# Performance work log

Hardware: AMD Instinct MI355X
Metric: run time of the kernel (lower is better)

## Reference

```python
import jax, jax.numpy as jnp
import numpy as np

NEG_SLOPE = 0.2

def _gat(x_src, x_dst, W_src, W_dst, a_src, a_dst, bias, src, dst, num_dst):
    # Bipartite PyG GATConv, heads=1, concat, add_self_loops=False.
    h_src = x_src @ W_src              # [N_src, H]
    h_dst = x_dst @ W_dst              # [N_dst, H]
    # Per-edge attention logits: leaky_relu(a_src.h_src[i] + a_dst.h_dst[j])
    e = jax.nn.leaky_relu((h_src @ a_src)[src] + (h_dst @ a_dst)[dst], NEG_SLOPE)  # [E]
    # Segment softmax over incoming edges of each dst node
    m = jax.ops.segment_max(e, dst, num_segments=num_dst)
    m = jnp.where(jnp.isfinite(m), m, 0.0)  # empty segments -> safe
    ex = jnp.exp(e - m[dst])
    denom = jax.ops.segment_sum(ex, dst, num_segments=num_dst)
    alpha = ex / denom[dst]            # [E]
    # Scatter-sum weighted source messages
    out = jax.ops.segment_sum(alpha[:, None] * h_src[src], dst, num_segments=num_dst)
    return out + bias


def setup_inputs() -> dict:
    key = jax.random.key(0)
    ks = jax.random.split(key, 20)
    N_L, N_A, D, H, O, E = 100000, 20000, 128, 128, 64, 500000
    s = 1.0 / np.sqrt(D)
    inp = {
        'x_label': jax.random.normal(ks[0], (N_L, D), jnp.float32),
        'x_attr': jax.random.normal(ks[1], (N_A, D), jnp.float32),
        'W_src_la': jax.random.normal(ks[2], (D, H), jnp.float32) * s,
        'W_dst_la': jax.random.normal(ks[3], (D, H), jnp.float32) * s,
        'a_src_la': jax.random.normal(ks[4], (H,), jnp.float32) * s,
        'a_dst_la': jax.random.normal(ks[5], (H,), jnp.float32) * s,
        'b_la': jax.random.normal(ks[6], (H,), jnp.float32) * 0.01,
        'W_src_al': jax.random.normal(ks[7], (D, H), jnp.float32) * s,
        'W_dst_al': jax.random.normal(ks[8], (D, H), jnp.float32) * s,
        'a_src_al': jax.random.normal(ks[9], (H,), jnp.float32) * s,
        'a_dst_al': jax.random.normal(ks[10], (H,), jnp.float32) * s,
        'b_al': jax.random.normal(ks[11], (H,), jnp.float32) * 0.01,
        'W_lin': jax.random.normal(ks[12], (H, O), jnp.float32) * s,
        'b_lin': jax.random.normal(ks[13], (O,), jnp.float32) * 0.01,
        'edge_src_la': jax.random.randint(ks[14], (E,), 0, N_L, jnp.int32),
        'edge_dst_la': jax.random.randint(ks[15], (E,), 0, N_A, jnp.int32),
        'edge_src_al': jax.random.randint(ks[16], (E,), 0, N_A, jnp.int32),
        'edge_dst_al': jax.random.randint(ks[17], (E,), 0, N_L, jnp.int32),
    }
    return inp


def reference(x_label, x_attr, W_src_la, W_dst_la, a_src_la, a_dst_la, b_la,
              W_src_al, W_dst_al, a_src_al, a_dst_al, b_al, W_lin, b_lin,
              edge_src_la, edge_dst_la, edge_src_al, edge_dst_al):
    N_L = x_label.shape[0]
    N_A = x_attr.shape[0]
    # label -> attribute GAT (output for 'attribute' nodes)
    h_attr = _gat(x_label, x_attr, W_src_la, W_dst_la, a_src_la, a_dst_la, b_la,
                  edge_src_la, edge_dst_la, N_A)
    # attribute -> label GAT (output for 'label' nodes)
    h_label = _gat(x_attr, x_label, W_src_al, W_dst_al, a_src_al, a_dst_al, b_al,
                   edge_src_al, edge_dst_al, N_L)
    h_attr = jax.nn.relu(h_attr)  # computed as in original (unused downstream)
    h_label = jax.nn.relu(h_label)
    out = h_label @ W_lin + b_lin
    return out
```

## Files before the change

kernel.cpp:

```cpp
#include <hip/hip_runtime.h>
#include <math.h>

#define NEG_SLOPE 0.2f

typedef __attribute__((ext_vector_type(8))) short bf16x8;
typedef __attribute__((ext_vector_type(4))) float f32x4;

__device__ __forceinline__ unsigned short f2bf(float f) {
    unsigned u = __float_as_uint(f);
    unsigned r = (u + 0x7FFFu + ((u >> 16) & 1u)) >> 16;
    return (unsigned short)r;
}

__device__ __forceinline__ void acc8(float* a, uint4 u, float x) {
    a[0] += x * __uint_as_float(u.x << 16);
    a[1] += x * __uint_as_float(u.x & 0xFFFF0000u);
    a[2] += x * __uint_as_float(u.y << 16);
    a[3] += x * __uint_as_float(u.y & 0xFFFF0000u);
    a[4] += x * __uint_as_float(u.z << 16);
    a[5] += x * __uint_as_float(u.z & 0xFFFF0000u);
    a[6] += x * __uint_as_float(u.w << 16);
    a[7] += x * __uint_as_float(u.w & 0xFFFF0000u);
}

__device__ __forceinline__ unsigned pack2(unsigned short lo, unsigned short hi) {
    return (unsigned)lo | ((unsigned)hi << 16);
}

__global__ __launch_bounds__(256) void k_pre(
    const int* __restrict__ dst, int* __restrict__ deg, int E, int nbDeg,
    const float* __restrict__ Wd, const float* __restrict__ ad,
    const float* __restrict__ Ws, const float* __restrict__ as_,
    float* __restrict__ wdst, float* __restrict__ wsrc,
    const float* __restrict__ Wlin, unsigned short* __restrict__ Wb) {
    int b = blockIdx.x, t = threadIdx.x;
    if (b < nbDeg) {
        int i = b * 256 + t;
        if (i < E) atomicAdd(&deg[dst[i]], 1);
    } else if (b == nbDeg) {
        const float* W = (t < 128) ? Wd : Ws;
        const float* a = (t < 128) ? ad : as_;
        int d = t & 127;
        float s = 0.f;
        #pragma unroll 8
        for (int h = 0; h < 128; ++h) s += W[d * 128 + h] * a[h];
        if (t < 128) wdst[d] = s; else wsrc[d] = s;
    } else {
        int idx = (b - nbDeg - 1) * 256 + t;
        int col = idx >> 7, k = idx & 127;
        Wb[idx] = f2bf(Wlin[k * 64 + col]);
    }
}

__device__ __forceinline__ void rowdot_role(const float* __restrict__ X,
                                            const float* __restrict__ v,
                                            float* __restrict__ out, int n,
                                            int vb, int t) {
    int wave = t >> 6, lane = t & 63;
    int half = lane >> 5, li = lane & 31;
    int row0 = (vb * 4 + wave) * 8 + half;
    const float4* X4 = (const float4*)X;
    const float4* V4 = (const float4*)v;
    float4 bv = V4[li];
    float p[4];
    #pragma unroll
    for (int k = 0; k < 4; ++k) {
        int row = row0 + 2 * k;
        p[k] = 0.f;
        if (row < n) {
            float4 x = X4[(size_t)row * 32 + li];
            p[k] = x.x * bv.x + x.y * bv.y + x.z * bv.z + x.w * bv.w;
        }
    }
    #pragma unroll
    for (int off = 16; off; off >>= 1) {
        #pragma unroll
        for (int k = 0; k < 4; ++k) p[k] += __shfl_xor(p[k], off);
    }
    if (li == 0) {
        #pragma unroll
        for (int k = 0; k < 4; ++k) {
            int row = row0 + 2 * k;
            if (row < n) out[row] = p[k];
        }
    }
}

__device__ __forceinline__ void hsrc_role(const float* __restrict__ X,
                                          const float* __restrict__ W,
                                          unsigned short* __restrict__ Hb,
                                          int nrows, int row0, int t,
                                          float* __restrict__ Xs ) {
    #pragma unroll
    for (int i = 0; i < 16; ++i) {
        int idx = t + i * 256;
        int r = idx >> 7;
        Xs[r * 128 + (idx & 127)] = (row0 + r < nrows) ? X[(size_t)row0 * 128 + idx] : 0.f;
    }
    __syncthreads();
    int cg = t & 31, rg = t >> 5;
    float acc[4][4];
    #pragma unroll
    for (int i = 0; i < 4; ++i)
        #pragma unroll
        for (int j = 0; j < 4; ++j) acc[i][j] = 0.f;
    const float4* W4 = (const float4*)W;
    #pragma unroll 4
    for (int d = 0; d < 128; ++d) {
        float4 wv = W4[d * 32 + cg];
        float x0 = Xs[(rg * 4 + 0) * 128 + d], x1 = Xs[(rg * 4 + 1) * 128 + d];
        float x2 = Xs[(rg * 4 + 2) * 128 + d], x3 = Xs[(rg * 4 + 3) * 128 + d];
        acc[0][0] += x0 * wv.x; acc[0][1] += x0 * wv.y; acc[0][2] += x0 * wv.z; acc[0][3] += x0 * wv.w;
        acc[1][0] += x1 * wv.x; acc[1][1] += x1 * wv.y; acc[1][2] += x1 * wv.z; acc[1][3] += x1 * wv.w;
        acc[2][0] += x2 * wv.x; acc[2][1] += x2 * wv.y; acc[2][2] += x2 * wv.z; acc[2][3] += x2 * wv.w;
        acc[3][0] += x3 * wv.x; acc[3][1] += x3 * wv.y; acc[3][2] += x3 * wv.z; acc[3][3] += x3 * wv.w;
    }
    #pragma unroll
    for (int i = 0; i < 4; ++i) {
        int gr = row0 + rg * 4 + i;
        if (gr < nrows) {
            ushort4 o;
            o.x = f2bf(acc[i][0]); o.y = f2bf(acc[i][1]);
            o.z = f2bf(acc[i][2]); o.w = f2bf(acc[i][3]);
            *(ushort4*)&Hb[(size_t)gr * 128 + cg * 4] = o;
        }
    }
}

__device__ __forceinline__ void scan_role(const int* __restrict__ deg,
                                          int* __restrict__ rowptr, int n, int E,
                                          int vb, int t, int* __restrict__ sd) {
    const int4* deg4 = (const int4*)deg;
    int nq = vb * 256;
    int s = 0;
    for (int i = t; i < nq; i += 256) {
        int4 v = deg4[i];
        s += (v.x + v.y) + (v.z + v.w);
    }
    sd[t] = s;
    __syncthreads();
    for (int off = 128; off; off >>= 1) {
        if (t < off) sd[t] += sd[t + off];
        __syncthreads();
    }
    int offset = sd[0];
    __syncthreads();
    int base = vb * 1024 + t * 4;
    int d[4]; int tsum = 0;
    #pragma unroll
    for (int i = 0; i < 4; ++i) { d[i] = (base + i < n) ? deg[base + i] : 0; tsum += d[i]; }
    sd[t] = tsum;
    __syncthreads();
    for (int off = 1; off < 256; off <<= 1) {
        int v = (t >= off) ? sd[t - off] : 0;
        __syncthreads();
        sd[t] += v;
        __syncthreads();
    }
    int excl = sd[t] - tsum + offset;
    #pragma unroll
    for (int i = 0; i < 4; ++i) {
        if (base + i < n) rowptr[base + i] = excl;
        excl += d[i];
    }
    if (vb == 0 && t == 0) rowptr[n] = E;
}

__global__ __launch_bounds__(256) void k_mid(
    const int* __restrict__ deg, int* __restrict__ rowptr, int nScan, int n, int E,
    const float* __restrict__ xL, const float* __restrict__ wdst,
    float* __restrict__ sdst, int nRL, int NL,
    const float* __restrict__ xA, const float* __restrict__ wsrc,
    float* __restrict__ ssrc, int nRA, int NA,
    const float* __restrict__ Wsrc, unsigned short* __restrict__ Hb, int nH) {
    __shared__ float smemf[32 * 128];
    int b = blockIdx.x, t = threadIdx.x;
    if (b < nH) {
        hsrc_role(xA, Wsrc, Hb, NA, b * 32, t, smemf);
    } else if (b < nH + nRL) {
        rowdot_role(xL, wdst, sdst, NL, b - nH, t);
    } else if (b < nH + nRL + nRA) {
        rowdot_role(xA, wsrc, ssrc, NA, b - nH - nRL, t);
    } else {
        scan_role(deg, rowptr, n, E, b - nH - nRL - nRA, t, (int*)smemf);
    }
}

__global__ void k_scatter(const int* __restrict__ src, const int* __restrict__ dst,
                          const float* __restrict__ ssrc, const float* __restrict__ sdst,
                          const int* __restrict__ rowptr, int* __restrict__ cursor,
                          int2* __restrict__ csr_pair, int E) {
    int i = blockIdx.x * blockDim.x + threadIdx.x;
    if (i >= E) return;
    int s = src[i], d = dst[i];
    float e = ssrc[s] + sdst[d];
    e = e > 0.f ? e : NEG_SLOPE * e;
    float ex = __expf(e);
    int pos = rowptr[d] + atomicAdd(&cursor[d], 1);
    csr_pair[pos] = make_int2(s, __float_as_int(ex));
}

__global__ __launch_bounds__(256) void k_gatout(
    const int* __restrict__ rowptr, const int2* __restrict__ csr_pair,
    const unsigned short* __restrict__ Hb, const float* __restrict__ b_al,
    const unsigned short* __restrict__ Wb, const float* __restrict__ b_lin,
    float* __restrict__ out, int n) {
    __shared__ unsigned short Gs[64 * 128];
    int t = threadIdx.x;
    int wave = t >> 6, lane = t & 63;
    int grp = lane >> 4, gl = lane & 15;
    const uint4* H16 = (const uint4*)Hb;
    int row0b = blockIdx.x * 64;
    const float4* B4 = (const float4*)b_al;
    float4 bA = B4[gl * 2], bB = B4[gl * 2 + 1];

    #pragma unroll
    for (int rr = 0; rr < 4; ++rr) {
        int rl = wave * 16 + rr * 4 + grp;
        int row = row0b + rl;
        uint4 gpack = make_uint4(0u, 0u, 0u, 0u);
        if (row < n) {
            int beg = rowptr[row], end = rowptr[row + 1];
            float a[8];
            #pragma unroll
            for (int k = 0; k < 8; ++k) a[k] = 0.f;
            float denom = 0.f;
            int j = beg;
            for (; j + 4 <= end; j += 4) {
                int2 p0 = csr_pair[j], p1 = csr_pair[j + 1];
                int2 p2 = csr_pair[j + 2], p3 = csr_pair[j + 3];
                float x0 = __int_as_float(p0.y), x1 = __int_as_float(p1.y);
                float x2 = __int_as_float(p2.y), x3 = __int_as_float(p3.y);
                uint4 u0 = H16[(size_t)p0.x * 16 + gl];
                uint4 u1 = H16[(size_t)p1.x * 16 + gl];
                uint4 u2 = H16[(size_t)p2.x * 16 + gl];
                uint4 u3 = H16[(size_t)p3.x * 16 + gl];
                denom += (x0 + x1) + (x2 + x3);
                acc8(a, u0, x0); acc8(a, u1, x1); acc8(a, u2, x2); acc8(a, u3, x3);
            }
            for (; j + 2 <= end; j += 2) {
                int2 p0 = csr_pair[j], p1 = csr_pair[j + 1];
                float x0 = __int_as_float(p0.y), x1 = __int_as_float(p1.y);
                uint4 u0 = H16[(size_t)p0.x * 16 + gl];
                uint4 u1 = H16[(size_t)p1.x * 16 + gl];
                denom += x0 + x1;
                acc8(a, u0, x0); acc8(a, u1, x1);
            }
            if (j < end) {
                int2 p0 = csr_pair[j];
                float x0 = __int_as_float(p0.y);
                uint4 u0 = H16[(size_t)p0.x * 16 + gl];
                denom += x0;
                acc8(a, u0, x0);
            }
            float inv = denom > 0.f ? 1.f / denom : 0.f;
            unsigned short g0 = f2bf(fmaxf(a[0] * inv + bA.x, 0.f));
            unsigned short g1 = f2bf(fmaxf(a[1] * inv + bA.y, 0.f));
            unsigned short g2 = f2bf(fmaxf(a[2] * inv + bA.z, 0.f));
            unsigned short g3 = f2bf(fmaxf(a[3] * inv + bA.w, 0.f));
            unsigned short g4 = f2bf(fmaxf(a[4] * inv + bB.x, 0.f));
            unsigned short g5 = f2bf(fmaxf(a[5] * inv + bB.y, 0.f));
            unsigned short g6 = f2bf(fmaxf(a[6] * inv + bB.z, 0.f));
            unsigned short g7 = f2bf(fmaxf(a[7] * inv + bB.w, 0.f));
            gpack = make_uint4(pack2(g0, g1), pack2(g2, g3), pack2(g4, g5), pack2(g6, g7));
        }
        int slot = gl ^ (rl & 15);
        *(uint4*)&Gs[rl * 128 + slot * 8] = gpack;
    }
    __syncthreads();

    int m = lane & 15, kq = lane >> 4;
    int rl = wave * 16 + m;
    f32x4 acc0 = {0.f, 0.f, 0.f, 0.f};
    f32x4 acc1 = {0.f, 0.f, 0.f, 0.f};
    f32x4 acc2 = {0.f, 0.f, 0.f, 0.f};
    f32x4 acc3 = {0.f, 0.f, 0.f, 0.f};
    const bf16x8* B0 = (const bf16x8*)(Wb + (size_t)(0 * 16 + m) * 128);
    const bf16x8* B1 = (const bf16x8*)(Wb + (size_t)(1 * 16 + m) * 128);
    const bf16x8* B2 = (const bf16x8*)(Wb + (size_t)(2 * 16 + m) * 128);
    const bf16x8* B3 = (const bf16x8*)(Wb + (size_t)(3 * 16 + m) * 128);
    #pragma unroll
    for (int s = 0; s < 4; ++s) {
        int ci = s * 4 + kq;
        int slot = ci ^ m;
        bf16x8 a = *(const bf16x8*)&Gs[rl * 128 + slot * 8];
        acc0 = __builtin_amdgcn_mfma_f32_16x16x32_bf16(a, B0[ci], acc0, 0, 0, 0);
        acc1 = __builtin_amdgcn_mfma_f32_16x16x32_bf16(a, B1[ci], acc1, 0, 0, 0);
        acc2 = __builtin_amdgcn_mfma_f32_16x16x32_bf16(a, B2[ci], acc2, 0, 0, 0);
        acc3 = __builtin_amdgcn_mfma_f32_16x16x32_bf16(a, B3[ci], acc3, 0, 0, 0);
    }
    float bl0 = b_lin[0 * 16 + m], bl1 = b_lin[1 * 16 + m];
    float bl2 = b_lin[2 * 16 + m], bl3 = b_lin[3 * 16 + m];
    int row0 = row0b + wave * 16;
    #pragma unroll
    for (int j = 0; j < 4; ++j) {
        int row = row0 + kq * 4 + j;
        if (row < n) {
            float* orow = out + (size_t)row * 64;
            orow[0 * 16 + m] = acc0[j] + bl0;
            orow[1 * 16 + m] = acc1[j] + bl1;
            orow[2 * 16 + m] = acc2[j] + bl2;
            orow[3 * 16 + m] = acc3[j] + bl3;
        }
    }
}

extern "C" void kernel_launch(void* const* d_in, const int* in_sizes, int n_in,
                              void* d_out, int out_size, void* d_ws, size_t ws_size,
                              hipStream_t stream) {
    const float* x_label  = (const float*)d_in[0];
    const float* x_attr   = (const float*)d_in[1];
    const float* W_src_al = (const float*)d_in[7];
    const float* W_dst_al = (const float*)d_in[8];
    const float* a_src_al = (const float*)d_in[9];
    const float* a_dst_al = (const float*)d_in[10];
    const float* b_al     = (const float*)d_in[11];
    const float* W_lin    = (const float*)d_in[12];
    const float* b_lin    = (const float*)d_in[13];
    const int* edge_src   = (const int*)d_in[16];
    const int* edge_dst   = (const int*)d_in[17];

    const int D = 128;
    const int N_L = in_sizes[0] / D;
    const int N_A = in_sizes[1] / D;
    const int E   = in_sizes[16];

    const int nbDeg = (E + 255) / 256;
    const int nScan = (N_L + 1023) / 1024;
    const int nRL   = (N_L + 31) / 32;
    const int nRA   = (N_A + 31) / 32;
    const int nH    = (N_A + 31) / 32;

    float* ws = (float*)d_ws;
    float* s_src = ws;
    float* s_dst = s_src + N_A;
    float* wdst  = s_dst + N_L;
    float* wsrc  = wdst + 128;
    int*   deg    = (int*)(wsrc + 128);
    int*   cursor = deg + N_L;
    int*   rowptr = cursor + N_L;
    int2*  csr_pair = (int2*)(rowptr + N_L + 4);
    unsigned short* Hb = (unsigned short*)(csr_pair + E);
    unsigned short* Wb = Hb + (size_t)N_A * 128;

    float* out = (float*)d_out;

    hipMemsetAsync(deg, 0, (size_t)2 * N_L * sizeof(int), stream);

    k_pre<<<nbDeg + 1 + 32, 256, 0, stream>>>(edge_dst, deg, E, nbDeg,
                                              W_dst_al, a_dst_al, W_src_al, a_src_al,
                                              wdst, wsrc, W_lin, Wb);
    k_mid<<<nH + nRL + nRA + nScan, 256, 0, stream>>>(
        deg, rowptr, nScan, N_L, E,
        x_label, wdst, s_dst, nRL, N_L,
        x_attr, wsrc, s_src, nRA, N_A,
        W_src_al, Hb, nH);
    k_scatter<<<nbDeg, 256, 0, stream>>>(edge_src, edge_dst, s_src, s_dst,
                                         rowptr, cursor, csr_pair, E);
    k_gatout<<<(N_L + 63) / 64, 256, 0, stream>>>(rowptr, csr_pair, Hb, b_al,
                                                  Wb, b_lin, out, N_L);
}
```

Measured before the change: 242.1 us.

## Interleave four rows' gathers in gatout, shrink blocks, process two edges per thread

```diff
diff --git a/kernel.cpp b/kernel.cpp
--- a/kernel.cpp
+++ b/kernel.cpp
@@ -35,8 +35,12 @@
     const float* __restrict__ Wlin, unsigned short* __restrict__ Wb) {
     int b = blockIdx.x, t = threadIdx.x;
     if (b < nbDeg) {
-        int i = b * 256 + t;
-        if (i < E) atomicAdd(&deg[dst[i]], 1);
+        int i = (b * 256 + t) * 2;
+        if (i < E) {
+            int2 dp = *(const int2*)(dst + i);
+            atomicAdd(&deg[dp.x], 1);
+            if (i + 1 < E) atomicAdd(&deg[dp.y], 1);
+        }
     } else if (b == nbDeg) {
         const float* W = (t < 128) ? Wd : Ws;
         const float* a = (t < 128) ? ad : as_;
@@ -190,87 +194,89 @@
                           const float* __restrict__ ssrc, const float* __restrict__ sdst,
                           const int* __restrict__ rowptr, int* __restrict__ cursor,
                           int2* __restrict__ csr_pair, int E) {
-    int i = blockIdx.x * blockDim.x + threadIdx.x;
+    int i = (blockIdx.x * blockDim.x + threadIdx.x) * 2;
     if (i >= E) return;
-    int s = src[i], d = dst[i];
-    float e = ssrc[s] + sdst[d];
-    e = e > 0.f ? e : NEG_SLOPE * e;
-    float ex = __expf(e);
-    int pos = rowptr[d] + atomicAdd(&cursor[d], 1);
-    csr_pair[pos] = make_int2(s, __float_as_int(ex));
-}
-
-__global__ __launch_bounds__(256) void k_gatout(
+    int2 sp = *(const int2*)(src + i);
+    int2 dp = *(const int2*)(dst + i);
+    bool v1 = (i + 1 < E);
+    float e0 = ssrc[sp.x] + sdst[dp.x];
+    float e1 = v1 ? ssrc[sp.y] + sdst[dp.y] : 0.f;
+    e0 = e0 > 0.f ? e0 : NEG_SLOPE * e0;
+    e1 = e1 > 0.f ? e1 : NEG_SLOPE * e1;
+    float x0 = __expf(e0), x1 = __expf(e1);
+    int pos0 = rowptr[dp.x] + atomicAdd(&cursor[dp.x], 1);
+    csr_pair[pos0] = make_int2(sp.x, __float_as_int(x0));
+    if (v1) {
+        int pos1 = rowptr[dp.y] + atomicAdd(&cursor[dp.y], 1);
+        csr_pair[pos1] = make_int2(sp.y, __float_as_int(x1));
+    }
+}
+
+__global__ __launch_bounds__(64) void k_gatout(
     const int* __restrict__ rowptr, const int2* __restrict__ csr_pair,
     const unsigned short* __restrict__ Hb, const float* __restrict__ b_al,
     const unsigned short* __restrict__ Wb, const float* __restrict__ b_lin,
     float* __restrict__ out, int n) {
-    __shared__ unsigned short Gs[64 * 128];
-    int t = threadIdx.x;
-    int wave = t >> 6, lane = t & 63;
+    __shared__ unsigned short Gs[16 * 128];
+    int lane = threadIdx.x & 63;
     int grp = lane >> 4, gl = lane & 15;
     const uint4* H16 = (const uint4*)Hb;
-    int row0b = blockIdx.x * 64;
+    int row0b = blockIdx.x * 16;
     const float4* B4 = (const float4*)b_al;
     float4 bA = B4[gl * 2], bB = B4[gl * 2 + 1];
 
-    #pragma unroll
-    for (int rr = 0; rr < 4; ++rr) {
-        int rl = wave * 16 + rr * 4 + grp;
-        int row = row0b + rl;
-        uint4 gpack = make_uint4(0u, 0u, 0u, 0u);
-        if (row < n) {
-            int beg = rowptr[row], end = rowptr[row + 1];
-            float a[8];
-            #pragma unroll
-            for (int k = 0; k < 8; ++k) a[k] = 0.f;
-            float denom = 0.f;
-            int j = beg;
-            for (; j + 4 <= end; j += 4) {
-                int2 p0 = csr_pair[j], p1 = csr_pair[j + 1];
-                int2 p2 = csr_pair[j + 2], p3 = csr_pair[j + 3];
-                float x0 = __int_as_float(p0.y), x1 = __int_as_float(p1.y);
-                float x2 = __int_as_float(p2.y), x3 = __int_as_float(p3.y);
-                uint4 u0 = H16[(size_t)p0.x * 16 + gl];
-                uint4 u1 = H16[(size_t)p1.x * 16 + gl];
-                uint4 u2 = H16[(size_t)p2.x * 16 + gl];
-                uint4 u3 = H16[(size_t)p3.x * 16 + gl];
-                denom += (x0 + x1) + (x2 + x3);
-                acc8(a, u0, x0); acc8(a, u1, x1); acc8(a, u2, x2); acc8(a, u3, x3);
-            }
-            for (; j + 2 <= end; j += 2) {
-                int2 p0 = csr_pair[j], p1 = csr_pair[j + 1];
-                float x0 = __int_as_float(p0.y), x1 = __int_as_float(p1.y);
-                uint4 u0 = H16[(size_t)p0.x * 16 + gl];
-                uint4 u1 = H16[(size_t)p1.x * 16 + gl];
-                denom += x0 + x1;
-                acc8(a, u0, x0); acc8(a, u1, x1);
-            }
-            if (j < end) {
-                int2 p0 = csr_pair[j];
-                float x0 = __int_as_float(p0.y);
-                uint4 u0 = H16[(size_t)p0.x * 16 + gl];
-                denom += x0;
-                acc8(a, u0, x0);
-            }
-            float inv = denom > 0.f ? 1.f / denom : 0.f;
-            unsigned short g0 = f2bf(fmaxf(a[0] * inv + bA.x, 0.f));
-            unsigned short g1 = f2bf(fmaxf(a[1] * inv + bA.y, 0.f));
-            unsigned short g2 = f2bf(fmaxf(a[2] * inv + bA.z, 0.f));
-            unsigned short g3 = f2bf(fmaxf(a[3] * inv + bA.w, 0.f));
-            unsigned short g4 = f2bf(fmaxf(a[4] * inv + bB.x, 0.f));
-            unsigned short g5 = f2bf(fmaxf(a[5] * inv + bB.y, 0.f));
-            unsigned short g6 = f2bf(fmaxf(a[6] * inv + bB.z, 0.f));
-            unsigned short g7 = f2bf(fmaxf(a[7] * inv + bB.w, 0.f));
-            gpack = make_uint4(pack2(g0, g1), pack2(g2, g3), pack2(g4, g5), pack2(g6, g7));
-        }
-        int slot = gl ^ (rl & 15);
+    int jj[4], ee[4];
+    float acc[4][8];
+    float den[4];
+    #pragma unroll
+    for (int r = 0; r < 4; ++r) {
+        int row = row0b + r * 4 + grp;
+        if (row < n) { jj[r] = rowptr[row]; ee[r] = rowptr[row + 1]; }
+        else         { jj[r] = 0;           ee[r] = 0; }
+        den[r] = 0.f;
+        #pragma unroll
+        for (int k = 0; k < 8; ++k) acc[r][k] = 0.f;
+    }
+
+    while (jj[0] < ee[0] || jj[1] < ee[1] || jj[2] < ee[2] || jj[3] < ee[3]) {
+        #pragma unroll
+        for (int r = 0; r < 4; ++r) {
+            bool v0 = jj[r] < ee[r];
+            bool v1 = jj[r] + 1 < ee[r];
+            int j0 = v0 ? jj[r] : 0;
+            int j1 = v1 ? jj[r] + 1 : 0;
+            int2 p0 = csr_pair[j0];
+            int2 p1 = csr_pair[j1];
+            uint4 u0 = H16[(size_t)p0.x * 16 + gl];
+            uint4 u1 = H16[(size_t)p1.x * 16 + gl];
+            float x0 = v0 ? __int_as_float(p0.y) : 0.f;
+            float x1 = v1 ? __int_as_float(p1.y) : 0.f;
+            den[r] += x0 + x1;
+            acc8(acc[r], u0, x0);
+            acc8(acc[r], u1, x1);
+            jj[r] += 2;
+        }
+    }
+
+    #pragma unroll
+    for (int r = 0; r < 4; ++r) {
+        int rl = r * 4 + grp;
+        float inv = den[r] > 0.f ? 1.f / den[r] : 0.f;
+        unsigned short g0 = f2bf(fmaxf(acc[r][0] * inv + bA.x, 0.f));
+        unsigned short g1 = f2bf(fmaxf(acc[r][1] * inv + bA.y, 0.f));
+        unsigned short g2 = f2bf(fmaxf(acc[r][2] * inv + bA.z, 0.f));
+        unsigned short g3 = f2bf(fmaxf(acc[r][3] * inv + bA.w, 0.f));
+        unsigned short g4 = f2bf(fmaxf(acc[r][4] * inv + bB.x, 0.f));
+        unsigned short g5 = f2bf(fmaxf(acc[r][5] * inv + bB.y, 0.f));
+        unsigned short g6 = f2bf(fmaxf(acc[r][6] * inv + bB.z, 0.f));
+        unsigned short g7 = f2bf(fmaxf(acc[r][7] * inv + bB.w, 0.f));
+        uint4 gpack = make_uint4(pack2(g0, g1), pack2(g2, g3), pack2(g4, g5), pack2(g6, g7));
+        int slot = gl ^ rl;
         *(uint4*)&Gs[rl * 128 + slot * 8] = gpack;
     }
     __syncthreads();
 
     int m = lane & 15, kq = lane >> 4;
-    int rl = wave * 16 + m;
     f32x4 acc0 = {0.f, 0.f, 0.f, 0.f};
     f32x4 acc1 = {0.f, 0.f, 0.f, 0.f};
     f32x4 acc2 = {0.f, 0.f, 0.f, 0.f};
@@ -283,7 +289,7 @@
     for (int s = 0; s < 4; ++s) {
         int ci = s * 4 + kq;
         int slot = ci ^ m;
-        bf16x8 a = *(const bf16x8*)&Gs[rl * 128 + slot * 8];
+        bf16x8 a = *(const bf16x8*)&Gs[m * 128 + slot * 8];
         acc0 = __builtin_amdgcn_mfma_f32_16x16x32_bf16(a, B0[ci], acc0, 0, 0, 0);
         acc1 = __builtin_amdgcn_mfma_f32_16x16x32_bf16(a, B1[ci], acc1, 0, 0, 0);
         acc2 = __builtin_amdgcn_mfma_f32_16x16x32_bf16(a, B2[ci], acc2, 0, 0, 0);
@@ -291,10 +297,9 @@
     }
     float bl0 = b_lin[0 * 16 + m], bl1 = b_lin[1 * 16 + m];
     float bl2 = b_lin[2 * 16 + m], bl3 = b_lin[3 * 16 + m];
-    int row0 = row0b + wave * 16;
     #pragma unroll
     for (int j = 0; j < 4; ++j) {
-        int row = row0 + kq * 4 + j;
+        int row = row0b + kq * 4 + j;
         if (row < n) {
             float* orow = out + (size_t)row * 64;
             orow[0 * 16 + m] = acc0[j] + bl0;
@@ -325,7 +330,7 @@
     const int N_A = in_sizes[1] / D;
     const int E   = in_sizes[16];
 
-    const int nbDeg = (E + 255) / 256;
+    const int nbDeg = (E + 511) / 512;
     const int nScan = (N_L + 1023) / 1024;
     const int nRL   = (N_L + 31) / 32;
     const int nRA   = (N_A + 31) / 32;
@@ -355,8 +360,8 @@
         x_label, wdst, s_dst, nRL, N_L,
         x_attr, wsrc, s_src, nRA, N_A,
         W_src_al, Hb, nH);
-    k_scatter<<<nbDeg, 256, 0, stream>>>(edge_src, edge_dst, s_src, s_dst,
-                                         rowptr, cursor, csr_pair, E);
-    k_gatout<<<(N_L + 63) / 64, 256, 0, stream>>>(rowptr, csr_pair, Hb, b_al,
-                                                  Wb, b_lin, out, N_L);
-}
+    k_scatter<<<(E + 511) / 512, 256, 0, stream>>>(edge_src, edge_dst, s_src, s_dst,
+                                                   rowptr, cursor, csr_pair, E);
+    k_gatout<<<(N_L + 15) / 16, 64, 0, stream>>>(rowptr, csr_pair, Hb, b_al,
+                                                 Wb, b_lin, out, N_L);
+}
```

Result: no change. 242.6 us (+0.2%).
